# Kernel tuning notes

Hardware: AMD Instinct MI355X
Metric: run time of the kernel (lower is better)

The kernel has to match this reference:

```python
import jax, jax.numpy as jnp
import numpy as np
from jax import lax

VOCAB, EMB, HID, TAGS = 50000, 300, 512, 50
T, B = 256, 64
H = HID // 2  # per-direction LSTM hidden


def _lstm(xs, W_ih, W_hh, b_ih, b_hh):
    # xs: [T, B, E]; PyTorch gate order i, f, g, o
    xp = jnp.einsum('tbe,ge->tbg', xs, W_ih) + b_ih  # precompute input projection

    def step(carry, x_t):
        h, c = carry
        gates = x_t + h @ W_hh.T + b_hh
        i, f, g, o = jnp.split(gates, 4, axis=-1)
        c = jax.nn.sigmoid(f) * c + jax.nn.sigmoid(i) * jnp.tanh(g)
        h = jax.nn.sigmoid(o) * jnp.tanh(c)
        return (h, c), h

    h0 = jnp.zeros((xs.shape[1], H), xs.dtype)
    _, hs = lax.scan(step, (h0, h0), xp)
    return hs  # [T, B, H]


def setup_inputs() -> dict:
    key = jax.random.key(0)
    ks = jax.random.split(key, 16)
    s_emb = 1.0
    s_lstm = 1.0 / np.sqrt(H)
    inp = {
        'x': jax.random.randint(ks[0], (T, B), 0, VOCAB),
        'y': jax.random.randint(ks[1], (T, B), 0, TAGS),
        'mask': jnp.ones((T, B), dtype=bool),
        'emb': jax.random.normal(ks[2], (VOCAB, EMB), jnp.float32) * s_emb,
        'W_ih_f': jax.random.uniform(ks[3], (4 * H, EMB), jnp.float32, -s_lstm, s_lstm),
        'W_hh_f': jax.random.uniform(ks[4], (4 * H, H), jnp.float32, -s_lstm, s_lstm),
        'b_ih_f': jax.random.uniform(ks[5], (4 * H,), jnp.float32, -s_lstm, s_lstm),
        'b_hh_f': jax.random.uniform(ks[6], (4 * H,), jnp.float32, -s_lstm, s_lstm),
        'W_ih_b': jax.random.uniform(ks[7], (4 * H, EMB), jnp.float32, -s_lstm, s_lstm),
        'W_hh_b': jax.random.uniform(ks[8], (4 * H, H), jnp.float32, -s_lstm, s_lstm),
        'b_ih_b': jax.random.uniform(ks[9], (4 * H,), jnp.float32, -s_lstm, s_lstm),
        'b_hh_b': jax.random.uniform(ks[10], (4 * H,), jnp.float32, -s_lstm, s_lstm),
        'W_out': jax.random.normal(ks[11], (TAGS, HID), jnp.float32) * 0.02,
        'b_out': jnp.zeros((TAGS,), jnp.float32),
        'start_trans': jax.random.uniform(ks[12], (TAGS,), jnp.float32, -0.1, 0.1),
        'end_trans': jax.random.uniform(ks[13], (TAGS,), jnp.float32, -0.1, 0.1),
        'trans': jax.random.uniform(ks[14], (TAGS, TAGS), jnp.float32, -0.1, 0.1),
    }
    return inp


def _emissions(x, emb, W_ih_f, W_hh_f, b_ih_f, b_hh_f, W_ih_b, W_hh_b, b_ih_b, b_hh_b, W_out, b_out):
    e = emb[x]                                   # [T, B, EMB]
    h_f = _lstm(e, W_ih_f, W_hh_f, b_ih_f, b_hh_f)
    h_b = _lstm(e[::-1], W_ih_b, W_hh_b, b_ih_b, b_hh_b)[::-1]
    h = jnp.concatenate([h_f, h_b], axis=-1)    # [T, B, HID]; dropout in eval mode = identity
    return jnp.einsum('tbh,kh->tbk', h, W_out) + b_out  # [T, B, TAGS]


def _crf_loss(em, y, mask, start_trans, end_trans, trans):
    maskf = mask.astype(em.dtype)
    tt = jnp.arange(1, T)
    bb = jnp.arange(B)
    # numerator: score of the gold path (torchcrf _compute_score)
    num = start_trans[y[0]] + em[0, bb, y[0]]
    num = num + (trans[y[:-1], y[1:]] * maskf[1:]).sum(0)
    num = num + (em[tt[:, None], bb[None, :], y[1:]] * maskf[1:]).sum(0)
    last_idx = mask.astype(jnp.int32).sum(0) - 1
    num = num + end_trans[y[last_idx, bb]]
    # denominator: forward algorithm (log-sum-exp DP)
    def fstep(score, inp):
        em_t, m_t = inp
        nxt = jax.nn.logsumexp(score[:, :, None] + trans[None] + em_t[:, None, :], axis=1)
        return jnp.where(m_t[:, None], nxt, score), None
    score0 = start_trans[None] + em[0]          # [B, TAGS]
    score, _ = lax.scan(fstep, score0, (em[1:], mask[1:]))
    denom = jax.nn.logsumexp(score + end_trans[None], axis=-1)
    return -(num - denom).sum()                 # loss = -llh (sum reduction)


def _crf_decode(em, mask, start_trans, end_trans, trans):
    def vstep(score, inp):
        em_t, m_t = inp
        combo = score[:, :, None] + trans[None]  # [B, prev, cur]
        idx = combo.argmax(1)
        nxt = combo.max(1) + em_t
        return jnp.where(m_t[:, None], nxt, score), idx
    score0 = start_trans[None] + em[0]
    score, history = lax.scan(vstep, score0, (em[1:], mask[1:]))  # history: [T-1, B, TAGS]
    last = jnp.argmax(score + end_trans[None], axis=-1)           # [B]
    def bstep(cur, inp):
        hist_t, m_t = inp
        prev = jnp.take_along_axis(hist_t, cur[:, None], axis=1)[:, 0]
        return jnp.where(m_t, prev, cur), cur
    tag0, rest = lax.scan(bstep, last, (history, mask[1:]), reverse=True)
    return jnp.concatenate([tag0[None], rest], axis=0)            # [T, B] int


def reference(x, y, mask, emb, W_ih_f, W_hh_f, b_ih_f, b_hh_f, W_ih_b, W_hh_b, b_ih_b, b_hh_b, W_out, b_out, start_trans, end_trans, trans):
    em = _emissions(x, emb, W_ih_f, W_hh_f, b_ih_f, b_hh_f, W_ih_b, W_hh_b, b_ih_b, b_hh_b, W_out, b_out)
    loss = _crf_loss(em, y, mask, start_trans, end_trans, trans)
    pred = _crf_decode(em, mask, start_trans, end_trans, trans)
    return (loss, pred)
```

## Files before the change

### kernel.cpp

```cpp
#include <hip/hip_runtime.h>
#include <math.h>

#define T_LEN 256
#define BATCH 64
#define NEMB  300
#define NHID  256
#define NG4   1024
#define NTAGS 50

typedef float    f32x4 __attribute__((ext_vector_type(4)));
typedef unsigned u32x4 __attribute__((ext_vector_type(4)));

static constexpr size_t XP_OFF  = 0;
static constexpr size_t XP_SZ   = (size_t)2 * 1024 * 16384;
static constexpr size_t HC_OFF  = XP_OFF + XP_SZ;
static constexpr size_t HC_SZ   = (size_t)T_LEN * 512 * 64;
static constexpr size_t HX_OFF  = HC_OFF + HC_SZ;
static constexpr size_t HX_SZ   = (size_t)2 * 2 * 256 * 64;
static constexpr size_t EM_OFF  = HX_OFF + HX_SZ;
static constexpr size_t EM_SZ   = (size_t)T_LEN * BATCH * NTAGS;
static constexpr size_t LLH_OFF = EM_OFF + EM_SZ;
static constexpr size_t FLG_OFF = LLH_OFF + 64;

__global__ __launch_bounds__(256)
void k_init(float* __restrict__ ws) {
    unsigned int* f = (unsigned int*)(ws + FLG_OFF);
    int i = blockIdx.x * 256 + threadIdx.x;
    if (i < 512) f[i] = 0u;
}

__global__ __launch_bounds__(256)
void k_xp(const int* __restrict__ x, const float* __restrict__ emb,
          const float* __restrict__ Wf, const float* __restrict__ Wb,
          const float* __restrict__ bihf, const float* __restrict__ bhhf,
          const float* __restrict__ bihb, const float* __restrict__ bhhb,
          float* __restrict__ xpT) {
    __shared__ float As[8 * 136];
    __shared__ float Ws[8 * 136];
    __shared__ int   xrow[128];

    const int tid  = threadIdx.x;
    const int row0 = blockIdx.x * 128;
    const int col0 = blockIdx.y * 128;
    const int dir  = col0 >> 10;
    const int g0   = col0 & 1023;
    const float* __restrict__ W   = dir ? Wb   : Wf;
    const float* __restrict__ bih = dir ? bihb : bihf;
    const float* __restrict__ bhh = dir ? bhhb : bhhf;

    if (tid < 128) xrow[tid] = x[row0 + tid];
    __syncthreads();

    float acc[8][8];
#pragma unroll
    for (int i = 0; i < 8; i++)
#pragma unroll
        for (int j = 0; j < 8; j++) acc[i][j] = 0.f;

    const int ty = tid >> 4;
    const int tx = tid & 15;

    for (int kc = 0; kc < NEMB; kc += 8) {
#pragma unroll
        for (int q = 0; q < 4; q++) {
            int idx = tid + 256 * q;
            int r   = idx >> 3;
            int kk  = idx & 7;
            int k   = kc + kk;
            float av = 0.f, wv = 0.f;
            if (k < NEMB) {
                av = emb[(size_t)xrow[r] * NEMB + k];
                wv = W[(size_t)(g0 + r) * NEMB + k];
            }
            As[kk * 136 + r] = av;
            Ws[kk * 136 + r] = wv;
        }
        __syncthreads();
#pragma unroll
        for (int kk = 0; kk < 8; kk++) {
            float4 a0 = *(const float4*)&As[kk * 136 + 8 * ty];
            float4 a1 = *(const float4*)&As[kk * 136 + 8 * ty + 4];
            float4 b0 = *(const float4*)&Ws[kk * 136 + 8 * tx];
            float4 b1 = *(const float4*)&Ws[kk * 136 + 8 * tx + 4];
            float a[8] = {a0.x,a0.y,a0.z,a0.w,a1.x,a1.y,a1.z,a1.w};
            float w[8] = {b0.x,b0.y,b0.z,b0.w,b1.x,b1.y,b1.z,b1.w};
#pragma unroll
            for (int i = 0; i < 8; i++)
#pragma unroll
                for (int j = 0; j < 8; j++) acc[i][j] += a[i] * w[j];
        }
        __syncthreads();
    }

#pragma unroll
    for (int jj = 0; jj < 8; jj++) {
        const int c = g0 + 8 * tx + jj;
        const float bb = bih[c] + bhh[c];
        float4 v0 = make_float4(acc[0][jj] + bb, acc[1][jj] + bb,
                                acc[2][jj] + bb, acc[3][jj] + bb);
        float4 v1 = make_float4(acc[4][jj] + bb, acc[5][jj] + bb,
                                acc[6][jj] + bb, acc[7][jj] + bb);
        float* dst = xpT + ((size_t)dir * 1024 + c) * 16384 + row0 + 8 * ty;
        *(float4*)dst       = v0;
        *(float4*)(dst + 4) = v1;
    }
}

__global__ __launch_bounds__(256, 1)
void k_lstm(const float* __restrict__ xpT, const float* __restrict__ Whf,
            const float* __restrict__ Whb, float* __restrict__ hcatT,
            float* __restrict__ hx, unsigned int* __restrict__ flg) {
    __shared__ float hs[BATCH * NHID];
    __shared__ float accS[8 * BATCH];

    const int wg    = blockIdx.x;
    const int dir   = wg >> 7;
    const int wslot = wg & 127;
    const int j0    = wslot * 2;
    const int tid   = threadIdx.x;
    const int w     = tid >> 6;
    const int lane  = tid & 63;
    const int rg    = w & 1;
    const int bhalf = w >> 1;
    const int kthr  = lane >> 3;
    const int bthr  = lane & 7;
    const int jme   = j0 + rg;

    const float* __restrict__ Wh  = dir ? Whb : Whf;
    const float* __restrict__ xpd = xpT + (size_t)dir * 1024 * 16384;
    float* __restrict__ hxd = hx + (size_t)dir * 32768;
    unsigned int* __restrict__ flgd = flg + dir * 128;

    float wreg[4][32];
#pragma unroll
    for (int g = 0; g < 4; ++g) {
        const float4* src = (const float4*)(Wh + ((size_t)(g * 256 + jme)) * 256 + kthr * 32);
#pragma unroll
        for (int q = 0; q < 8; ++q) {
            float4 v = src[q];
            wreg[g][q * 4 + 0] = v.x;
            wreg[g][q * 4 + 1] = v.y;
            wreg[g][q * 4 + 2] = v.z;
            wreg[g][q * 4 + 3] = v.w;
        }
    }
    float creg[2] = {0.f, 0.f};

    for (int s = 0; s < T_LEN; ++s) {
        const int t = dir ? (T_LEN - 1 - s) : s;

        float xq[2][4];
        if (w == 0) {
#pragma unroll
            for (int jj = 0; jj < 2; ++jj)
#pragma unroll
                for (int g = 0; g < 4; ++g)
                    xq[jj][g] = xpd[((size_t)(g * 256 + j0 + jj)) * 16384 + t * 64 + lane];
        }

        float acc[4][4];
#pragma unroll
        for (int g = 0; g < 4; ++g)
#pragma unroll
            for (int bi = 0; bi < 4; ++bi) acc[g][bi] = 0.f;

        if (s > 0) {
            const unsigned sU = (unsigned)s;
            if (lane < 32) {
                const unsigned int* fp = flgd + lane * 4;
                while (true) {
                    u32x4 f;
                    asm volatile("global_load_dwordx4 %0, %1, off sc0 sc1\n\t"
                                 "s_waitcnt vmcnt(0)"
                                 : "=v"(f) : "v"(fp) : "memory");
                    if (f.x >= sU && f.y >= sU && f.z >= sU && f.w >= sU) break;
                    __builtin_amdgcn_s_sleep(1);
                }
            }

            const float* hsrc = hxd + (size_t)((s - 1) & 1) * 16384;
            const int b0   = (tid & 15) * 4;
            const int rot4 = 4 * (tid & 7);
#pragma unroll
            for (int h8 = 0; h8 < 2; ++h8) {
                f32x4 stv[8];
#pragma unroll
                for (int q = 0; q < 8; ++q) {
                    const float* ap = hsrc + (h8 * 8 + q) * 1024 + tid * 4;
                    asm volatile("global_load_dwordx4 %0, %1, off sc0 sc1"
                                 : "=v"(stv[q]) : "v"(ap));
                }
                asm volatile("s_waitcnt vmcnt(0)" ::: "memory");
#pragma unroll
                for (int q = 0; q < 8; ++q) {
                    const int kk = (h8 * 8 + q) * 16 + (tid >> 4);
                    const int sw = (kk & ~31) | ((kk + rot4) & 31);
                    hs[(b0 + 0) * 256 + sw] = stv[q].x;
                    hs[(b0 + 1) * 256 + sw] = stv[q].y;
                    hs[(b0 + 2) * 256 + sw] = stv[q].z;
                    hs[(b0 + 3) * 256 + sw] = stv[q].w;
                }
            }
            __syncthreads();

#pragma unroll
            for (int bi = 0; bi < 4; ++bi) {
                const int b = bhalf * 32 + bthr * 4 + bi;
                const float* hb = &hs[b * 256 + kthr * 32];
                const int rot = bthr;
#pragma unroll
                for (int c8 = 0; c8 < 8; ++c8) {
                    const float4 h4 = *(const float4*)&hb[4 * ((c8 + rot) & 7)];
#pragma unroll
                    for (int g = 0; g < 4; ++g) {
                        acc[g][bi] += h4.x * wreg[g][4 * c8 + 0]
                                    + h4.y * wreg[g][4 * c8 + 1]
                                    + h4.z * wreg[g][4 * c8 + 2]
                                    + h4.w * wreg[g][4 * c8 + 3];
                    }
                }
            }
#pragma unroll
            for (int g = 0; g < 4; ++g)
#pragma unroll
                for (int bi = 0; bi < 4; ++bi) {
                    float v = acc[g][bi];
                    v += __shfl_xor(v, 8);
                    v += __shfl_xor(v, 16);
                    v += __shfl_xor(v, 32);
                    acc[g][bi] = v;
                }
            if (kthr == 0) {
#pragma unroll
                for (int g = 0; g < 4; ++g) {
                    float4 v = make_float4(acc[g][0], acc[g][1], acc[g][2], acc[g][3]);
                    *(float4*)&accS[(rg * 4 + g) * 64 + bhalf * 32 + bthr * 4] = v;
                }
            }
            __syncthreads();
        }

        if (w == 0) {
#pragma unroll
            for (int jj = 0; jj < 2; ++jj) {
                float gi = xq[jj][0], gf = xq[jj][1], gg = xq[jj][2], go = xq[jj][3];
                if (s > 0) {
                    gi += accS[(jj * 4 + 0) * 64 + lane];
                    gf += accS[(jj * 4 + 1) * 64 + lane];
                    gg += accS[(jj * 4 + 2) * 64 + lane];
                    go += accS[(jj * 4 + 3) * 64 + lane];
                }
                float ig = 1.f / (1.f + expf(-gi));
                float fg = 1.f / (1.f + expf(-gf));
                float tg = tanhf(gg);
                float og = 1.f / (1.f + expf(-go));
                float cn = fg * creg[jj] + ig * tg;
                creg[jj] = cn;
                float hv = og * tanhf(cn);
                hcatT[(size_t)t * 32768 + (size_t)(dir * 256 + j0 + jj) * 64 + lane] = hv;
                float* hp = &hxd[(size_t)(s & 1) * 16384 + (j0 + jj) * 64 + lane];
                asm volatile("global_store_dword %0, %1, off sc0 sc1"
                             :: "v"(hp), "v"(hv) : "memory");
            }
            if (s < T_LEN - 1) {
                asm volatile("s_waitcnt vmcnt(0)" ::: "memory");
                if (lane == 0) {
                    unsigned sv = (unsigned)(s + 1);
                    asm volatile("global_store_dword %0, %1, off sc0 sc1"
                                 :: "v"(&flgd[wslot]), "v"(sv) : "memory");
                }
            }
        }
    }
}

__global__ __launch_bounds__(256)
void k_em(const float* __restrict__ hcatT, const float* __restrict__ Wout,
          const float* __restrict__ bout, float* __restrict__ em) {
    __shared__ float Ws[52 * 132];
    __shared__ float ht[128 * 64];
    const int t   = blockIdx.x;
    const int tid = threadIdx.x;
    const int b   = tid & 63;
    const int tg  = tid >> 6;
    const int tagbase = tg * 13;

    float acc[13];
#pragma unroll
    for (int i = 0; i < 13; i++) acc[i] = 0.f;

    for (int k0 = 0; k0 < 512; k0 += 128) {
        __syncthreads();
#pragma unroll
        for (int q = 0; q < 25; q++) {
            int idx = tid + 256 * q;
            if (idx < 6400) {
                int tag = idx >> 7, kk = idx & 127;
                Ws[tag * 132 + kk] = Wout[(size_t)tag * 512 + k0 + kk];
            }
        }
#pragma unroll
        for (int q = 0; q < 32; q++) {
            int idx = tid + 256 * q;
            ht[idx] = hcatT[(size_t)t * 32768 + (size_t)k0 * 64 + idx];
        }
        __syncthreads();
        for (int kk = 0; kk < 128; kk++) {
            float hv = ht[kk * 64 + b];
#pragma unroll
            for (int i = 0; i < 13; i++)
                acc[i] += hv * Ws[(tagbase + i) * 132 + kk];
        }
    }
#pragma unroll
    for (int i = 0; i < 13; i++) {
        int tag = tagbase + i;
        if (tag < NTAGS)
            em[((size_t)t * BATCH + b) * NTAGS + tag] = acc[i] + bout[tag];
    }
}

__global__ __launch_bounds__(64)
void k_crf_loss(const float* __restrict__ em, const int* __restrict__ y,
                const float* __restrict__ st, const float* __restrict__ et,
                const float* __restrict__ tr, float* __restrict__ llh) {
    __shared__ float trs[2500];
    __shared__ float score[NTAGS];
    __shared__ float red[64];
    const int b   = blockIdx.x;
    const int tid = threadIdx.x;

#pragma unroll
    for (int q = 0; q < 40; q++) {
        int idx = tid + 64 * q;
        if (idx < 2500) trs[idx] = tr[idx];
    }
    __syncthreads();

    float part = 0.f;
    for (int t = tid; t < T_LEN; t += 64) {
        int yt = y[t * BATCH + b];
        if (t == 0) {
            part += st[yt] + em[(size_t)b * NTAGS + yt];
        } else {
            int yp = y[(t - 1) * BATCH + b];
            part += trs[yp * NTAGS + yt] + em[((size_t)t * BATCH + b) * NTAGS + yt];
        }
    }
    red[tid] = part;
    __syncthreads();
    for (int off = 32; off > 0; off >>= 1) {
        if (tid < off) red[tid] += red[tid + off];
        __syncthreads();
    }

    if (tid < NTAGS) score[tid] = st[tid] + em[(size_t)b * NTAGS + tid];
    __syncthreads();

    for (int t = 1; t < T_LEN; t++) {
        float ns = 0.f;
        if (tid < NTAGS) {
            float m = -1e30f;
            for (int p = 0; p < NTAGS; p++) {
                float v = score[p] + trs[p * NTAGS + tid];
                m = fmaxf(m, v);
            }
            float ssum = 0.f;
            for (int p = 0; p < NTAGS; p++) {
                float v = score[p] + trs[p * NTAGS + tid];
                ssum += expf(v - m);
            }
            ns = m + logf(ssum) + em[((size_t)t * BATCH + b) * NTAGS + tid];
        }
        __syncthreads();
        if (tid < NTAGS) score[tid] = ns;
        __syncthreads();
    }

    if (tid == 0) {
        float m = -1e30f;
        for (int cc = 0; cc < NTAGS; cc++) m = fmaxf(m, score[cc] + et[cc]);
        float ssum = 0.f;
        for (int cc = 0; cc < NTAGS; cc++) ssum += expf(score[cc] + et[cc] - m);
        float denom = m + logf(ssum);
        float num = red[0] + et[y[(T_LEN - 1) * BATCH + b]];
        llh[b] = num - denom;
    }
}

__global__ __launch_bounds__(64)
void k_viterbi(const float* __restrict__ em, const float* __restrict__ st,
               const float* __restrict__ et, const float* __restrict__ tr,
               float* __restrict__ out) {
    __shared__ float trs[2500];
    __shared__ float score[NTAGS];
    __shared__ unsigned char hist[(T_LEN - 1) * NTAGS];
    const int b   = blockIdx.x;
    const int tid = threadIdx.x;

#pragma unroll
    for (int q = 0; q < 40; q++) {
        int idx = tid + 64 * q;
        if (idx < 2500) trs[idx] = tr[idx];
    }
    if (tid < NTAGS) score[tid] = st[tid] + em[(size_t)b * NTAGS + tid];
    __syncthreads();

    for (int t = 1; t < T_LEN; t++) {
        float ns = 0.f;
        int am = 0;
        if (tid < NTAGS) {
            float m = -1e30f;
            for (int p = 0; p < NTAGS; p++) {
                float v = score[p] + trs[p * NTAGS + tid];
                if (v > m) { m = v; am = p; }
            }
            ns = m + em[((size_t)t * BATCH + b) * NTAGS + tid];
        }
        __syncthreads();
        if (tid < NTAGS) {
            score[tid] = ns;
            hist[(t - 1) * NTAGS + tid] = (unsigned char)am;
        }
        __syncthreads();
    }

    if (tid == 0) {
        float m = -1e30f;
        int cur = 0;
        for (int cc = 0; cc < NTAGS; cc++) {
            float v = score[cc] + et[cc];
            if (v > m) { m = v; cur = cc; }
        }
        out[1 + (T_LEN - 1) * BATCH + b] = (float)cur;
        for (int t = T_LEN - 2; t >= 0; t--) {
            cur = hist[t * NTAGS + cur];
            out[1 + t * BATCH + b] = (float)cur;
        }
    }
}

__global__ __launch_bounds__(64)
void k_loss_final(const float* __restrict__ llh, float* __restrict__ out) {
    __shared__ float red[64];
    const int tid = threadIdx.x;
    red[tid] = llh[tid];
    __syncthreads();
    for (int off = 32; off > 0; off >>= 1) {
        if (tid < off) red[tid] += red[tid + off];
        __syncthreads();
    }
    if (tid == 0) out[0] = -red[0];
}

extern "C" void kernel_launch(void* const* d_in, const int* in_sizes, int n_in,
                              void* d_out, int out_size, void* d_ws, size_t ws_size,
                              hipStream_t stream) {
    const int*   x    = (const int*)d_in[0];
    const int*   y    = (const int*)d_in[1];
    const float* emb  = (const float*)d_in[3];
    const float* Wihf = (const float*)d_in[4];
    const float* Whhf = (const float*)d_in[5];
    const float* bihf = (const float*)d_in[6];
    const float* bhhf = (const float*)d_in[7];
    const float* Wihb = (const float*)d_in[8];
    const float* Whhb = (const float*)d_in[9];
    const float* bihb = (const float*)d_in[10];
    const float* bhhb = (const float*)d_in[11];
    const float* Wout = (const float*)d_in[12];
    const float* bout = (const float*)d_in[13];
    const float* st   = (const float*)d_in[14];
    const float* et   = (const float*)d_in[15];
    const float* tr   = (const float*)d_in[16];

    float* out  = (float*)d_out;
    float* ws   = (float*)d_ws;
    float* xpT  = ws + XP_OFF;
    float* hcatT= ws + HC_OFF;
    float* hx   = ws + HX_OFF;
    float* em   = ws + EM_OFF;
    float* llh  = ws + LLH_OFF;
    unsigned int* flg = (unsigned int*)(ws + FLG_OFF);

    hipLaunchKernelGGL(k_init, dim3(2), dim3(256), 0, stream, ws);

    dim3 g1(128, 16);
    hipLaunchKernelGGL(k_xp, g1, dim3(256), 0, stream,
                       x, emb, Wihf, Wihb, bihf, bhhf, bihb, bhhb, xpT);

    hipLaunchKernelGGL(k_lstm, dim3(256), dim3(256), 0, stream,
                       xpT, Whhf, Whhb, hcatT, hx, flg);

    hipLaunchKernelGGL(k_em, dim3(T_LEN), dim3(256), 0, stream, hcatT, Wout, bout, em);

    hipLaunchKernelGGL(k_crf_loss, dim3(BATCH), dim3(64), 0, stream, em, y, st, et, tr, llh);

    hipLaunchKernelGGL(k_viterbi, dim3(BATCH), dim3(64), 0, stream, em, st, et, tr, out);

    hipLaunchKernelGGL(k_loss_final, dim3(1), dim3(64), 0, stream, llh, out);
}
```

Measured before the change: 4.291 ms.

## Replace per-block flag polling with per-step atomic counters in LSTM

The cross-workgroup barrier in the recurrent LSTM kernel changes. Before, 32 lanes polled 128 per-block step flags; now each block atomically increments a per-step counter and a single thread spins until it reaches 128, then releases the block with __syncthreads. The hidden-state gather also issues all 16 vector loads up front and waits in two halves, so the latency of the second half of the loads overlaps with the first half's LDS writes. This should make each polling round cheaper, at the cost of contention on one counter address and a longer sleep interval that may add wake-up latency.

```diff
diff --git a/kernel.cpp b/kernel.cpp
--- a/kernel.cpp
+++ b/kernel.cpp
@@ -9,7 +9,6 @@
 #define NTAGS 50
 
 typedef float    f32x4 __attribute__((ext_vector_type(4)));
-typedef unsigned u32x4 __attribute__((ext_vector_type(4)));
 
 static constexpr size_t XP_OFF  = 0;
 static constexpr size_t XP_SZ   = (size_t)2 * 1024 * 16384;
@@ -20,11 +19,11 @@
 static constexpr size_t EM_OFF  = HX_OFF + HX_SZ;
 static constexpr size_t EM_SZ   = (size_t)T_LEN * BATCH * NTAGS;
 static constexpr size_t LLH_OFF = EM_OFF + EM_SZ;
-static constexpr size_t FLG_OFF = LLH_OFF + 64;
+static constexpr size_t CNT_OFF = LLH_OFF + 64;
 
 __global__ __launch_bounds__(256)
 void k_init(float* __restrict__ ws) {
-    unsigned int* f = (unsigned int*)(ws + FLG_OFF);
+    unsigned int* f = (unsigned int*)(ws + CNT_OFF);
     int i = blockIdx.x * 256 + threadIdx.x;
     if (i < 512) f[i] = 0u;
 }
@@ -109,7 +108,7 @@
 __global__ __launch_bounds__(256, 1)
 void k_lstm(const float* __restrict__ xpT, const float* __restrict__ Whf,
             const float* __restrict__ Whb, float* __restrict__ hcatT,
-            float* __restrict__ hx, unsigned int* __restrict__ flg) {
+            float* __restrict__ hx, unsigned int* __restrict__ cnt) {
     __shared__ float hs[BATCH * NHID];
     __shared__ float accS[8 * BATCH];
 
@@ -129,7 +128,7 @@
     const float* __restrict__ Wh  = dir ? Whb : Whf;
     const float* __restrict__ xpd = xpT + (size_t)dir * 1024 * 16384;
     float* __restrict__ hxd = hx + (size_t)dir * 32768;
-    unsigned int* __restrict__ flgd = flg + dir * 128;
+    unsigned int* __restrict__ cntd = cnt + dir * 256;
 
     float wreg[4][32];
 #pragma unroll
@@ -165,41 +164,43 @@
             for (int bi = 0; bi < 4; ++bi) acc[g][bi] = 0.f;
 
         if (s > 0) {
-            const unsigned sU = (unsigned)s;
-            if (lane < 32) {
-                const unsigned int* fp = flgd + lane * 4;
-                while (true) {
-                    u32x4 f;
-                    asm volatile("global_load_dwordx4 %0, %1, off sc0 sc1\n\t"
-                                 "s_waitcnt vmcnt(0)"
-                                 : "=v"(f) : "v"(fp) : "memory");
-                    if (f.x >= sU && f.y >= sU && f.z >= sU && f.w >= sU) break;
-                    __builtin_amdgcn_s_sleep(1);
+            if (tid == 0) {
+                while (__hip_atomic_load(&cntd[s - 1], __ATOMIC_RELAXED,
+                                         __HIP_MEMORY_SCOPE_AGENT) < 128u) {
+                    __builtin_amdgcn_s_sleep(4);
                 }
             }
+            __syncthreads();
 
             const float* hsrc = hxd + (size_t)((s - 1) & 1) * 16384;
+            f32x4 stv[16];
+#pragma unroll
+            for (int q = 0; q < 16; ++q) {
+                const float* ap = hsrc + q * 1024 + tid * 4;
+                asm volatile("global_load_dwordx4 %0, %1, off sc0 sc1"
+                             : "=v"(stv[q]) : "v"(ap));
+            }
             const int b0   = (tid & 15) * 4;
             const int rot4 = 4 * (tid & 7);
-#pragma unroll
-            for (int h8 = 0; h8 < 2; ++h8) {
-                f32x4 stv[8];
-#pragma unroll
-                for (int q = 0; q < 8; ++q) {
-                    const float* ap = hsrc + (h8 * 8 + q) * 1024 + tid * 4;
-                    asm volatile("global_load_dwordx4 %0, %1, off sc0 sc1"
-                                 : "=v"(stv[q]) : "v"(ap));
-                }
-                asm volatile("s_waitcnt vmcnt(0)" ::: "memory");
-#pragma unroll
-                for (int q = 0; q < 8; ++q) {
-                    const int kk = (h8 * 8 + q) * 16 + (tid >> 4);
-                    const int sw = (kk & ~31) | ((kk + rot4) & 31);
-                    hs[(b0 + 0) * 256 + sw] = stv[q].x;
-                    hs[(b0 + 1) * 256 + sw] = stv[q].y;
-                    hs[(b0 + 2) * 256 + sw] = stv[q].z;
-                    hs[(b0 + 3) * 256 + sw] = stv[q].w;
-                }
+            asm volatile("s_waitcnt vmcnt(8)" ::: "memory");
+#pragma unroll
+            for (int q = 0; q < 8; ++q) {
+                const int kk = q * 16 + (tid >> 4);
+                const int sw = (kk & ~31) | ((kk + rot4) & 31);
+                hs[(b0 + 0) * 256 + sw] = stv[q].x;
+                hs[(b0 + 1) * 256 + sw] = stv[q].y;
+                hs[(b0 + 2) * 256 + sw] = stv[q].z;
+                hs[(b0 + 3) * 256 + sw] = stv[q].w;
+            }
+            asm volatile("s_waitcnt vmcnt(0)" ::: "memory");
+#pragma unroll
+            for (int q = 8; q < 16; ++q) {
+                const int kk = q * 16 + (tid >> 4);
+                const int sw = (kk & ~31) | ((kk + rot4) & 31);
+                hs[(b0 + 0) * 256 + sw] = stv[q].x;
+                hs[(b0 + 1) * 256 + sw] = stv[q].y;
+                hs[(b0 + 2) * 256 + sw] = stv[q].z;
+                hs[(b0 + 3) * 256 + sw] = stv[q].w;
             }
             __syncthreads();
 
@@ -265,9 +266,8 @@
             if (s < T_LEN - 1) {
                 asm volatile("s_waitcnt vmcnt(0)" ::: "memory");
                 if (lane == 0) {
-                    unsigned sv = (unsigned)(s + 1);
-                    asm volatile("global_store_dword %0, %1, off sc0 sc1"
-                                 :: "v"(&flgd[wslot]), "v"(sv) : "memory");
+                    __hip_atomic_fetch_add(&cntd[s], 1u, __ATOMIC_RELAXED,
+                                           __HIP_MEMORY_SCOPE_AGENT);
                 }
             }
         }
@@ -480,7 +480,7 @@
     float* hx   = ws + HX_OFF;
     float* em   = ws + EM_OFF;
     float* llh  = ws + LLH_OFF;
-    unsigned int* flg = (unsigned int*)(ws + FLG_OFF);
+    unsigned int* cnt = (unsigned int*)(ws + CNT_OFF);
 
     hipLaunchKernelGGL(k_init, dim3(2), dim3(256), 0, stream, ws);
 
@@ -489,7 +489,7 @@
                        x, emb, Wihf, Wihb, bihf, bhhf, bihb, bhhb, xpT);
 
     hipLaunchKernelGGL(k_lstm, dim3(256), dim3(256), 0, stream,
-                       xpT, Whhf, Whhb, hcatT, hx, flg);
+                       xpT, Whhf, Whhb, hcatT, hx, cnt);
 
     hipLaunchKernelGGL(k_em, dim3(T_LEN), dim3(256), 0, stream, hcatT, Wout, bout, em);
 
```

After: 3.475 ms. 19.0% less time.
